# Kernel tuning notes

Measured on AMD Instinct MI355X. Metric: run time of the kernel, lower is better.

Reference implementation:

```python
import jax, jax.numpy as jnp
import numpy as np

N, K, D = 8192, 256, 64

def setup_inputs() -> dict:
    key = jax.random.key(0)
    k1, k2, k3, k4, k5 = jax.random.split(key, 5)
    x = jax.random.normal(k1, (N, D), dtype=jnp.float32)
    means = 0.001 * jax.random.uniform(k2, (K, D), dtype=jnp.float32)
    diag = jax.random.normal(k3, (1, K, D), dtype=jnp.float32)
    tri = 0.01 * jax.random.normal(k4, (1, K, D, D), dtype=jnp.float32)
    weigh = jax.random.normal(k5, (1, K), dtype=jnp.float32)
    return {"x": x, "means": means, "diag": diag, "tri": tri, "weigh": weigh}

def reference(x, means, diag, tri, weigh):
    d = x.shape[1]
    logC = -d / 2 * jnp.log(jnp.asarray(2 * np.pi, dtype=x.dtype))
    w = jax.nn.log_softmax(weigh, axis=1)                 # [1,K]
    y = x[:, None, :] - means[None, :, :]                 # [N,K,d]
    lv = jnp.tanh(diag)                                   # [1,K,d]
    y = y * lv                                            # [N,K,d]
    L = jnp.tril(tri[0], k=-1)                            # [K,d,d] strictly lower
    y = y + jnp.einsum('kij,nkj->nki', L, y)              # [N,K,d]
    q = jnp.sum(y * y, axis=2)                            # [N,K]
    logdet = jnp.sum(jnp.log(jnp.abs(lv)), axis=2)        # [1,K]
    val = -q / 2 + logdet + w                             # [N,K]
    logpdf = logC + jax.nn.logsumexp(val, axis=-1)        # [N]
    return jnp.mean(-logpdf)                              # scalar
```

## Files before the change

kernel.cpp:

```cpp
#include <hip/hip_runtime.h>
#include <cstdint>
#include <cstddef>

#define NTOT 8192
#define KTOT 256

typedef _Float16 half2v __attribute__((ext_vector_type(2)));
typedef _Float16 half8  __attribute__((ext_vector_type(8)));
typedef float floatx16 __attribute__((ext_vector_type(16)));

static constexpr size_t G_ELEMS   = (size_t)8 * 260 * 64 * 8;
static constexpr size_t OFF_CK    = G_ELEMS * 2;
static constexpr size_t OFF_BPART = OFF_CK + 1024;
static constexpr size_t OFF_VAL   = 2134016;

__device__ __forceinline__ uint16_t f2h(float x) {
  _Float16 h = (_Float16)x;
  return __builtin_bit_cast(uint16_t, h);
}

__device__ __forceinline__ half8 mkh(half2v s, const half2v* rp) {
  union { half2v p[4]; half8 v; } u;
  u.p[0] = s * rp[0]; u.p[1] = s * rp[1]; u.p[2] = s * rp[2]; u.p[3] = s * rp[3];
  return u.v;
}
__device__ __forceinline__ half8 cph(const half2v* rp) {
  union { half2v p[4]; half8 v; } u;
  u.p[0] = rp[0]; u.p[1] = rp[1]; u.p[2] = rp[2]; u.p[3] = rp[3];
  return u.v;
}

__global__ void p1_prep(const float* __restrict__ means, const float* __restrict__ diag,
                        const float* __restrict__ tri, const float* __restrict__ weigh,
                        uint16_t* __restrict__ Gf, float* __restrict__ ck) {
  int k = blockIdx.x;
  int t = threadIdx.x;
  __shared__ float lv[64], ms[64], bv64[64], wred[256];
  __shared__ float Wp[64][68];
  __shared__ float SS[64][65];
  __shared__ float lse_s;

  float wv = weigh[t];
  wred[t] = wv; __syncthreads();
  for (int o = 128; o > 0; o >>= 1) { if (t < o) wred[t] = fmaxf(wred[t], wred[t + o]); __syncthreads(); }
  float wm = wred[0]; __syncthreads();
  wred[t] = __expf(wv - wm); __syncthreads();
  for (int o = 128; o > 0; o >>= 1) { if (t < o) wred[t] += wred[t + o]; __syncthreads(); }
  if (t == 0) lse_s = wm + __logf(wred[0]);

  float logdet0 = 0.f;
  if (t < 64) {
    float d = diag[k * 64 + t];
    float l = tanhf(d);
    lv[t] = l;
    ms[t] = means[k * 64 + t];
    float ld = __logf(fabsf(l));
    #pragma unroll
    for (int o = 32; o > 0; o >>= 1) ld += __shfl_xor(ld, o);
    logdet0 = ld;
  }
  __syncthreads();

  for (int e = 0; e < 16; ++e) {
    int idx = e * 256 + t;
    int i = idx >> 6, c = idx & 63;
    float L = (c < i) ? tri[k * 4096 + idx] : 0.f;
    float w = ((c == i) ? 1.f : 0.f) + L;
    Wp[i][c] = w * lv[c];
  }
  __syncthreads();

  int i0 = (t >> 4) * 4, j0 = (t & 15) * 4;
  float acc[4][4];
  #pragma unroll
  for (int a = 0; a < 4; ++a)
    #pragma unroll
    for (int b = 0; b < 4; ++b) acc[a][b] = 0.f;
  for (int r = 0; r < 64; ++r) {
    float4 av = *(const float4*)&Wp[r][i0];
    float4 bv = *(const float4*)&Wp[r][j0];
    float aa[4] = {av.x, av.y, av.z, av.w};
    float bb[4] = {bv.x, bv.y, bv.z, bv.w};
    #pragma unroll
    for (int a = 0; a < 4; ++a)
      #pragma unroll
      for (int b = 0; b < 4; ++b) acc[a][b] = fmaf(aa[a], bb[b], acc[a][b]);
  }
  #pragma unroll
  for (int a = 0; a < 4; ++a)
    #pragma unroll
    for (int b = 0; b < 4; ++b) SS[i0 + a][j0 + b] = acc[a][b];
  __syncthreads();

  if (t < 64) {
    float b = 0.f;
    for (int j = 0; j < 64; ++j) b = fmaf(SS[t][j], ms[j], b);
    bv64[t] = b;
    float bm = b * ms[t];
    #pragma unroll
    for (int o = 32; o > 0; o >>= 1) bm += __shfl_xor(bm, o);
    if (t == 0) ck[k] = logdet0 + (weigh[k] - lse_s) - 0.5f * bm;
  }
  __syncthreads();

  int k32 = k >> 5, kl = k & 31;
  for (int cc = t; cc < 520; cc += 256) {
    float v[8];
    if (cc < 512) {
      int i = cc >> 3, jb = (cc & 7) * 8;
      #pragma unroll
      for (int e = 0; e < 8; ++e) v[e] = -0.5f * SS[i][jb + e];
    } else {
      int b0 = (cc - 512) * 8;
      #pragma unroll
      for (int e = 0; e < 8; ++e) v[e] = bv64[b0 + e];
    }
    uint4 pk;
    pk.x = (uint32_t)f2h(v[0]) | ((uint32_t)f2h(v[1]) << 16);
    pk.y = (uint32_t)f2h(v[2]) | ((uint32_t)f2h(v[3]) << 16);
    pk.z = (uint32_t)f2h(v[4]) | ((uint32_t)f2h(v[5]) << 16);
    pk.w = (uint32_t)f2h(v[6]) | ((uint32_t)f2h(v[7]) << 16);
    size_t base = ((size_t)(k32 * 260 + (cc >> 1)) * 64 + (cc & 1) * 32 + kl) * 8;
    *(uint4*)(Gf + base) = pk;
  }
}

__launch_bounds__(256)
__global__ void k2_gemm(const float* __restrict__ x, const uint16_t* __restrict__ Gf,
                        const float* __restrict__ ck, float* __restrict__ val2) {
  __shared__ float xl[128][65];
  int t = threadIdx.x;
  int bx = blockIdx.x, by = blockIdx.y;
  const float* xblk = x + (size_t)bx * (128 * 64);

  for (int e = 0; e < 8; ++e) {
    int lin = e * 1024 + t * 4;
    float4 v = *(const float4*)(xblk + lin);
    int r = lin >> 6, c = lin & 63;
    xl[r][c] = v.x; xl[r][c + 1] = v.y; xl[r][c + 2] = v.z; xl[r][c + 3] = v.w;
  }
  __syncthreads();

  int wave = t >> 6, l = t & 63;
  int wn = wave >> 1, wk = wave & 1;
  int half = l >> 5, lane31 = l & 31;
  int r0 = wn * 64 + lane31, r1 = r0 + 32;

  half2v runh0[4][4], runh1[4][4];
  #pragma unroll
  for (int c = 0; c < 4; ++c) {
    int base = c * 16 + half * 8;
    float4 ra = *(const float4*)(xblk + (size_t)r0 * 64 + base);
    float4 rb = *(const float4*)(xblk + (size_t)r0 * 64 + base + 4);
    runh0[c][0][0] = (_Float16)ra.x; runh0[c][0][1] = (_Float16)ra.y;
    runh0[c][1][0] = (_Float16)ra.z; runh0[c][1][1] = (_Float16)ra.w;
    runh0[c][2][0] = (_Float16)rb.x; runh0[c][2][1] = (_Float16)rb.y;
    runh0[c][3][0] = (_Float16)rb.z; runh0[c][3][1] = (_Float16)rb.w;
    float4 rc = *(const float4*)(xblk + (size_t)r1 * 64 + base);
    float4 rd = *(const float4*)(xblk + (size_t)r1 * 64 + base + 4);
    runh1[c][0][0] = (_Float16)rc.x; runh1[c][0][1] = (_Float16)rc.y;
    runh1[c][1][0] = (_Float16)rc.z; runh1[c][1][1] = (_Float16)rc.w;
    runh1[c][2][0] = (_Float16)rd.x; runh1[c][2][1] = (_Float16)rd.y;
    runh1[c][3][0] = (_Float16)rd.z; runh1[c][3][1] = (_Float16)rd.w;
  }

  int k32 = by * 2 + wk;
  const uint4* Bp = (const uint4*)Gf;
  size_t bofs = (size_t)(k32 * 260) * 64 + l;

  floatx16 acc0, acc1;
  #pragma unroll
  for (int i = 0; i < 16; ++i) { acc0[i] = 0.f; acc1[i] = 0.f; }

  uint4 bufs[4][4];
  #pragma unroll
  for (int p = 0; p < 4; ++p)
    #pragma unroll
    for (int c = 0; c < 4; ++c) bufs[p][c] = Bp[bofs + (size_t)(p * 4 + c) * 64];

  for (int g = 0; g < 64; g += 4) {
    #pragma unroll
    for (int p = 0; p < 4; ++p) {
      int gg = g + p;
      float xf0 = xl[r0][gg], xf1 = xl[r1][gg];
      _Float16 h0 = (_Float16)xf0; half2v xi0; xi0[0] = h0; xi0[1] = h0;
      _Float16 h1 = (_Float16)xf1; half2v xi1; xi1[0] = h1; xi1[1] = h1;
      #pragma unroll
      for (int c = 0; c < 4; ++c) {
        half8 a0 = mkh(xi0, runh0[c]);
        half8 a1 = mkh(xi1, runh1[c]);
        half8 bb = __builtin_bit_cast(half8, bufs[p][c]);
        acc0 = __builtin_amdgcn_mfma_f32_32x32x16_f16(a0, bb, acc0, 0, 0, 0);
        acc1 = __builtin_amdgcn_mfma_f32_32x32x16_f16(a1, bb, acc1, 0, 0, 0);
      }
      #pragma unroll
      for (int c = 0; c < 4; ++c)
        bufs[p][c] = Bp[bofs + (size_t)((gg + 4) * 4 + c) * 64];
    }
  }

  #pragma unroll
  for (int c = 0; c < 4; ++c) {
    half8 a0 = cph(runh0[c]);
    half8 a1 = cph(runh1[c]);
    half8 bb = __builtin_bit_cast(half8, bufs[0][c]);
    acc0 = __builtin_amdgcn_mfma_f32_32x32x16_f16(a0, bb, acc0, 0, 0, 0);
    acc1 = __builtin_amdgcn_mfma_f32_32x32x16_f16(a1, bb, acc1, 0, 0, 0);
  }

  __syncthreads();
  float ckv = ck[by * 64 + wk * 32 + lane31];
  #pragma unroll
  for (int reg = 0; reg < 16; ++reg) {
    int row = (reg & 3) + 8 * (reg >> 2) + 4 * half;
    xl[wn * 64 + row][wk * 32 + lane31] = acc0[reg] + ckv;
    xl[wn * 64 + 32 + row][wk * 32 + lane31] = acc1[reg] + ckv;
  }
  __syncthreads();
  if (t < 128) {
    float m = -3.0e38f;
    #pragma unroll
    for (int j = 0; j < 64; ++j) m = fmaxf(m, xl[t][j]);
    float s = 0.f;
    #pragma unroll
    for (int j = 0; j < 64; ++j) s += __expf(xl[t][j] - m);
    size_t n = (size_t)bx * 128 + t;
    val2[n * 8 + by * 2 + 0] = m;
    val2[n * 8 + by * 2 + 1] = s;
  }
}

__global__ void k3_lse(const float* __restrict__ val2, float* __restrict__ bpart) {
  __shared__ float red[4];
  int t = threadIdx.x;
  size_t n = (size_t)blockIdx.x * 256 + t;
  const float4* p = (const float4*)(val2 + n * 8);
  float4 a = p[0], b = p[1];
  float M = fmaxf(fmaxf(a.x, a.z), fmaxf(b.x, b.z));
  float s = a.y * __expf(a.x - M) + a.w * __expf(a.z - M) +
            b.y * __expf(b.x - M) + b.w * __expf(b.z - M);
  float lse = M + __logf(s);
  #pragma unroll
  for (int o = 32; o > 0; o >>= 1) lse += __shfl_xor(lse, o);
  if ((t & 63) == 0) red[t >> 6] = lse;
  __syncthreads();
  if (t == 0) bpart[blockIdx.x] = red[0] + red[1] + red[2] + red[3];
}

__global__ void k4_final(const float* __restrict__ bpart, float* __restrict__ out) {
  int t = threadIdx.x;
  float v = (t < 32) ? bpart[t] : 0.f;
  #pragma unroll
  for (int o = 32; o > 0; o >>= 1) v += __shfl_xor(v, o);
  if (t == 0) out[0] = 58.8120661251f - v / 8192.0f;
}

extern "C" void kernel_launch(void* const* d_in, const int* in_sizes, int n_in,
                              void* d_out, int out_size, void* d_ws, size_t ws_size,
                              hipStream_t stream) {
  const float* x     = (const float*)d_in[0];
  const float* means = (const float*)d_in[1];
  const float* diag  = (const float*)d_in[2];
  const float* tri   = (const float*)d_in[3];
  const float* weigh = (const float*)d_in[4];

  char* ws = (char*)d_ws;
  uint16_t* Gf  = (uint16_t*)ws;
  float* ck     = (float*)(ws + OFF_CK);
  float* bpart  = (float*)(ws + OFF_BPART);
  float* val2   = (float*)(ws + OFF_VAL);

  p1_prep<<<dim3(256), dim3(256), 0, stream>>>(means, diag, tri, weigh, Gf, ck);
  k2_gemm<<<dim3(64, 4), dim3(256), 0, stream>>>(x, Gf, ck, val2);
  k3_lse<<<dim3(32), dim3(256), 0, stream>>>(val2, bpart);
  k4_final<<<dim3(1), dim3(64), 0, stream>>>(bpart, (float*)d_out);
}
```

Measured before the change: 97.95 us.

## Fuse all four kernels into one cooperative kernel with grid sync and last-block reduction

Merges the prep, GEMM/logsumexp, per-row LSE and final reduction kernels into a single cooperative launch of 256 blocks. A grid-wide sync separates the parameter preparation from the GEMM phase. A ticketed atomic counter lets the last finishing block do the final reduction. This removes three kernel launches and their inter-kernel gaps, at the cost of grid-sync overhead and higher LDS use per block, since both stages' shared arrays now coexist. The counter is reset by block 0 within the same launch, which relies on ordering that the grid sync provides.

After: 160.1 us. 1.64x slower.

```diff
diff --git a/kernel.cpp b/kernel.cpp
--- a/kernel.cpp
+++ b/kernel.cpp
@@ -1,6 +1,9 @@
 #include <hip/hip_runtime.h>
+#include <hip/hip_cooperative_groups.h>
 #include <cstdint>
 #include <cstddef>
+
+namespace cg = cooperative_groups;
 
 #define NTOT 8192
 #define KTOT 256
@@ -11,7 +14,7 @@
 
 static constexpr size_t G_ELEMS   = (size_t)8 * 260 * 64 * 8;
 static constexpr size_t OFF_CK    = G_ELEMS * 2;
-static constexpr size_t OFF_BPART = OFF_CK + 1024;
+static constexpr size_t OFF_CNT   = OFF_CK + 1024;
 static constexpr size_t OFF_VAL   = 2134016;
 
 __device__ __forceinline__ uint16_t f2h(float x) {
@@ -30,229 +33,237 @@
   return u.v;
 }
 
-__global__ void p1_prep(const float* __restrict__ means, const float* __restrict__ diag,
-                        const float* __restrict__ tri, const float* __restrict__ weigh,
-                        uint16_t* __restrict__ Gf, float* __restrict__ ck) {
-  int k = blockIdx.x;
-  int t = threadIdx.x;
+__launch_bounds__(256)
+__global__ void fused(const float* __restrict__ x, const float* __restrict__ means,
+                      const float* __restrict__ diag, const float* __restrict__ tri,
+                      const float* __restrict__ weigh, uint16_t* __restrict__ Gf,
+                      float* __restrict__ ck, float* __restrict__ val2,
+                      unsigned int* __restrict__ counter, float* __restrict__ out) {
   __shared__ float lv[64], ms[64], bv64[64], wred[256];
   __shared__ float Wp[64][68];
   __shared__ float SS[64][65];
   __shared__ float lse_s;
-
-  float wv = weigh[t];
-  wred[t] = wv; __syncthreads();
-  for (int o = 128; o > 0; o >>= 1) { if (t < o) wred[t] = fmaxf(wred[t], wred[t + o]); __syncthreads(); }
-  float wm = wred[0]; __syncthreads();
-  wred[t] = __expf(wv - wm); __syncthreads();
-  for (int o = 128; o > 0; o >>= 1) { if (t < o) wred[t] += wred[t + o]; __syncthreads(); }
-  if (t == 0) lse_s = wm + __logf(wred[0]);
-
-  float logdet0 = 0.f;
-  if (t < 64) {
-    float d = diag[k * 64 + t];
-    float l = tanhf(d);
-    lv[t] = l;
-    ms[t] = means[k * 64 + t];
-    float ld = __logf(fabsf(l));
-    #pragma unroll
-    for (int o = 32; o > 0; o >>= 1) ld += __shfl_xor(ld, o);
-    logdet0 = ld;
+  __shared__ float xl[128][65];
+  __shared__ int ticket_s;
+
+  int t = threadIdx.x;
+
+  {
+    int k = blockIdx.x;
+    if (k == 0 && t == 0) *counter = 0;
+
+    float wv = weigh[t];
+    wred[t] = wv; __syncthreads();
+    for (int o = 128; o > 0; o >>= 1) { if (t < o) wred[t] = fmaxf(wred[t], wred[t + o]); __syncthreads(); }
+    float wm = wred[0]; __syncthreads();
+    wred[t] = __expf(wv - wm); __syncthreads();
+    for (int o = 128; o > 0; o >>= 1) { if (t < o) wred[t] += wred[t + o]; __syncthreads(); }
+    if (t == 0) lse_s = wm + __logf(wred[0]);
+
+    float logdet0 = 0.f;
+    if (t < 64) {
+      float d = diag[k * 64 + t];
+      float l = tanhf(d);
+      lv[t] = l;
+      ms[t] = means[k * 64 + t];
+      float ld = __logf(fabsf(l));
+      #pragma unroll
+      for (int o = 32; o > 0; o >>= 1) ld += __shfl_xor(ld, o);
+      logdet0 = ld;
+    }
+    __syncthreads();
+
+    for (int e = 0; e < 16; ++e) {
+      int idx = e * 256 + t;
+      int i = idx >> 6, c = idx & 63;
+      float L = (c < i) ? tri[k * 4096 + idx] : 0.f;
+      float w = ((c == i) ? 1.f : 0.f) + L;
+      Wp[i][c] = w * lv[c];
+    }
+    __syncthreads();
+
+    int i0 = (t >> 4) * 4, j0 = (t & 15) * 4;
+    float acc[4][4];
+    #pragma unroll
+    for (int a = 0; a < 4; ++a)
+      #pragma unroll
+      for (int b = 0; b < 4; ++b) acc[a][b] = 0.f;
+    for (int r = 0; r < 64; ++r) {
+      float4 av = *(const float4*)&Wp[r][i0];
+      float4 bv = *(const float4*)&Wp[r][j0];
+      float aa[4] = {av.x, av.y, av.z, av.w};
+      float bb[4] = {bv.x, bv.y, bv.z, bv.w};
+      #pragma unroll
+      for (int a = 0; a < 4; ++a)
+        #pragma unroll
+        for (int b = 0; b < 4; ++b) acc[a][b] = fmaf(aa[a], bb[b], acc[a][b]);
+    }
+    #pragma unroll
+    for (int a = 0; a < 4; ++a)
+      #pragma unroll
+      for (int b = 0; b < 4; ++b) SS[i0 + a][j0 + b] = acc[a][b];
+    __syncthreads();
+
+    if (t < 64) {
+      float b = 0.f;
+      for (int j = 0; j < 64; ++j) b = fmaf(SS[t][j], ms[j], b);
+      bv64[t] = b;
+      float bm = b * ms[t];
+      #pragma unroll
+      for (int o = 32; o > 0; o >>= 1) bm += __shfl_xor(bm, o);
+      if (t == 0) ck[k] = logdet0 + (weigh[k] - lse_s) - 0.5f * bm;
+    }
+    __syncthreads();
+
+    int k32 = k >> 5, kl = k & 31;
+    for (int cc = t; cc < 520; cc += 256) {
+      float v[8];
+      if (cc < 512) {
+        int i = cc >> 3, jb = (cc & 7) * 8;
+        #pragma unroll
+        for (int e = 0; e < 8; ++e) v[e] = -0.5f * SS[i][jb + e];
+      } else {
+        int b0 = (cc - 512) * 8;
+        #pragma unroll
+        for (int e = 0; e < 8; ++e) v[e] = bv64[b0 + e];
+      }
+      uint4 pk;
+      pk.x = (uint32_t)f2h(v[0]) | ((uint32_t)f2h(v[1]) << 16);
+      pk.y = (uint32_t)f2h(v[2]) | ((uint32_t)f2h(v[3]) << 16);
+      pk.z = (uint32_t)f2h(v[4]) | ((uint32_t)f2h(v[5]) << 16);
+      pk.w = (uint32_t)f2h(v[6]) | ((uint32_t)f2h(v[7]) << 16);
+      size_t base = ((size_t)(k32 * 260 + (cc >> 1)) * 64 + (cc & 1) * 32 + kl) * 8;
+      *(uint4*)(Gf + base) = pk;
+    }
+  }
+
+  cg::this_grid().sync();
+
+  {
+    int bx = blockIdx.x >> 2, by = blockIdx.x & 3;
+    const float* xblk = x + (size_t)bx * (128 * 64);
+
+    for (int e = 0; e < 8; ++e) {
+      int lin = e * 1024 + t * 4;
+      float4 v = *(const float4*)(xblk + lin);
+      int r = lin >> 6, c = lin & 63;
+      xl[r][c] = v.x; xl[r][c + 1] = v.y; xl[r][c + 2] = v.z; xl[r][c + 3] = v.w;
+    }
+    __syncthreads();
+
+    int wave = t >> 6, l = t & 63;
+    int wn = wave >> 1, wk = wave & 1;
+    int half = l >> 5, lane31 = l & 31;
+    int r0 = wn * 64 + lane31, r1 = r0 + 32;
+
+    half2v runh0[4][4], runh1[4][4];
+    #pragma unroll
+    for (int c = 0; c < 4; ++c) {
+      int base = c * 16 + half * 8;
+      float4 ra = *(const float4*)(xblk + (size_t)r0 * 64 + base);
+      float4 rb = *(const float4*)(xblk + (size_t)r0 * 64 + base + 4);
+      runh0[c][0][0] = (_Float16)ra.x; runh0[c][0][1] = (_Float16)ra.y;
+      runh0[c][1][0] = (_Float16)ra.z; runh0[c][1][1] = (_Float16)ra.w;
+      runh0[c][2][0] = (_Float16)rb.x; runh0[c][2][1] = (_Float16)rb.y;
+      runh0[c][3][0] = (_Float16)rb.z; runh0[c][3][1] = (_Float16)rb.w;
+      float4 rc = *(const float4*)(xblk + (size_t)r1 * 64 + base);
+      float4 rd = *(const float4*)(xblk + (size_t)r1 * 64 + base + 4);
+      runh1[c][0][0] = (_Float16)rc.x; runh1[c][0][1] = (_Float16)rc.y;
+      runh1[c][1][0] = (_Float16)rc.z; runh1[c][1][1] = (_Float16)rc.w;
+      runh1[c][2][0] = (_Float16)rd.x; runh1[c][2][1] = (_Float16)rd.y;
+      runh1[c][3][0] = (_Float16)rd.z; runh1[c][3][1] = (_Float16)rd.w;
+    }
+
+    int k32 = by * 2 + wk;
+    const uint4* Bp = (const uint4*)Gf;
+    size_t bofs = (size_t)(k32 * 260) * 64 + l;
+
+    floatx16 acc0, acc1;
+    #pragma unroll
+    for (int i = 0; i < 16; ++i) { acc0[i] = 0.f; acc1[i] = 0.f; }
+
+    uint4 bufs[4][4];
+    #pragma unroll
+    for (int p = 0; p < 4; ++p)
+      #pragma unroll
+      for (int c = 0; c < 4; ++c) bufs[p][c] = Bp[bofs + (size_t)(p * 4 + c) * 64];
+
+    for (int g = 0; g < 64; g += 4) {
+      #pragma unroll
+      for (int p = 0; p < 4; ++p) {
+        int gg = g + p;
+        float xf0 = xl[r0][gg], xf1 = xl[r1][gg];
+        _Float16 h0 = (_Float16)xf0; half2v xi0; xi0[0] = h0; xi0[1] = h0;
+        _Float16 h1 = (_Float16)xf1; half2v xi1; xi1[0] = h1; xi1[1] = h1;
+        #pragma unroll
+        for (int c = 0; c < 4; ++c) {
+          half8 a0 = mkh(xi0, runh0[c]);
+          half8 a1 = mkh(xi1, runh1[c]);
+          half8 bb = __builtin_bit_cast(half8, bufs[p][c]);
+          acc0 = __builtin_amdgcn_mfma_f32_32x32x16_f16(a0, bb, acc0, 0, 0, 0);
+          acc1 = __builtin_amdgcn_mfma_f32_32x32x16_f16(a1, bb, acc1, 0, 0, 0);
+        }
+        #pragma unroll
+        for (int c = 0; c < 4; ++c)
+          bufs[p][c] = Bp[bofs + (size_t)((gg + 4) * 4 + c) * 64];
+      }
+    }
+
+    #pragma unroll
+    for (int c = 0; c < 4; ++c) {
+      half8 a0 = cph(runh0[c]);
+      half8 a1 = cph(runh1[c]);
+      half8 bb = __builtin_bit_cast(half8, bufs[0][c]);
+      acc0 = __builtin_amdgcn_mfma_f32_32x32x16_f16(a0, bb, acc0, 0, 0, 0);
+      acc1 = __builtin_amdgcn_mfma_f32_32x32x16_f16(a1, bb, acc1, 0, 0, 0);
+    }
+
+    __syncthreads();
+    float ckv = ck[by * 64 + wk * 32 + lane31];
+    #pragma unroll
+    for (int reg = 0; reg < 16; ++reg) {
+      int row = (reg & 3) + 8 * (reg >> 2) + 4 * half;
+      xl[wn * 64 + row][wk * 32 + lane31] = acc0[reg] + ckv;
+      xl[wn * 64 + 32 + row][wk * 32 + lane31] = acc1[reg] + ckv;
+    }
+    __syncthreads();
+    if (t < 128) {
+      float m = -3.0e38f;
+      #pragma unroll
+      for (int j = 0; j < 64; ++j) m = fmaxf(m, xl[t][j]);
+      float s = 0.f;
+      #pragma unroll
+      for (int j = 0; j < 64; ++j) s += __expf(xl[t][j] - m);
+      size_t n = (size_t)bx * 128 + t;
+      val2[n * 8 + by * 2 + 0] = m;
+      val2[n * 8 + by * 2 + 1] = s;
+    }
+    __syncthreads();
+  }
+
+  if (t == 0) {
+    __threadfence();
+    ticket_s = (int)atomicAdd(counter, 1u);
   }
   __syncthreads();
-
-  for (int e = 0; e < 16; ++e) {
-    int idx = e * 256 + t;
-    int i = idx >> 6, c = idx & 63;
-    float L = (c < i) ? tri[k * 4096 + idx] : 0.f;
-    float w = ((c == i) ? 1.f : 0.f) + L;
-    Wp[i][c] = w * lv[c];
-  }
-  __syncthreads();
-
-  int i0 = (t >> 4) * 4, j0 = (t & 15) * 4;
-  float acc[4][4];
-  #pragma unroll
-  for (int a = 0; a < 4; ++a)
-    #pragma unroll
-    for (int b = 0; b < 4; ++b) acc[a][b] = 0.f;
-  for (int r = 0; r < 64; ++r) {
-    float4 av = *(const float4*)&Wp[r][i0];
-    float4 bv = *(const float4*)&Wp[r][j0];
-    float aa[4] = {av.x, av.y, av.z, av.w};
-    float bb[4] = {bv.x, bv.y, bv.z, bv.w};
-    #pragma unroll
-    for (int a = 0; a < 4; ++a)
-      #pragma unroll
-      for (int b = 0; b < 4; ++b) acc[a][b] = fmaf(aa[a], bb[b], acc[a][b]);
-  }
-  #pragma unroll
-  for (int a = 0; a < 4; ++a)
-    #pragma unroll
-    for (int b = 0; b < 4; ++b) SS[i0 + a][j0 + b] = acc[a][b];
-  __syncthreads();
-
-  if (t < 64) {
-    float b = 0.f;
-    for (int j = 0; j < 64; ++j) b = fmaf(SS[t][j], ms[j], b);
-    bv64[t] = b;
-    float bm = b * ms[t];
-    #pragma unroll
-    for (int o = 32; o > 0; o >>= 1) bm += __shfl_xor(bm, o);
-    if (t == 0) ck[k] = logdet0 + (weigh[k] - lse_s) - 0.5f * bm;
-  }
-  __syncthreads();
-
-  int k32 = k >> 5, kl = k & 31;
-  for (int cc = t; cc < 520; cc += 256) {
-    float v[8];
-    if (cc < 512) {
-      int i = cc >> 3, jb = (cc & 7) * 8;
-      #pragma unroll
-      for (int e = 0; e < 8; ++e) v[e] = -0.5f * SS[i][jb + e];
-    } else {
-      int b0 = (cc - 512) * 8;
-      #pragma unroll
-      for (int e = 0; e < 8; ++e) v[e] = bv64[b0 + e];
-    }
-    uint4 pk;
-    pk.x = (uint32_t)f2h(v[0]) | ((uint32_t)f2h(v[1]) << 16);
-    pk.y = (uint32_t)f2h(v[2]) | ((uint32_t)f2h(v[3]) << 16);
-    pk.z = (uint32_t)f2h(v[4]) | ((uint32_t)f2h(v[5]) << 16);
-    pk.w = (uint32_t)f2h(v[6]) | ((uint32_t)f2h(v[7]) << 16);
-    size_t base = ((size_t)(k32 * 260 + (cc >> 1)) * 64 + (cc & 1) * 32 + kl) * 8;
-    *(uint4*)(Gf + base) = pk;
-  }
-}
-
-__launch_bounds__(256)
-__global__ void k2_gemm(const float* __restrict__ x, const uint16_t* __restrict__ Gf,
-                        const float* __restrict__ ck, float* __restrict__ val2) {
-  __shared__ float xl[128][65];
-  int t = threadIdx.x;
-  int bx = blockIdx.x, by = blockIdx.y;
-  const float* xblk = x + (size_t)bx * (128 * 64);
-
-  for (int e = 0; e < 8; ++e) {
-    int lin = e * 1024 + t * 4;
-    float4 v = *(const float4*)(xblk + lin);
-    int r = lin >> 6, c = lin & 63;
-    xl[r][c] = v.x; xl[r][c + 1] = v.y; xl[r][c + 2] = v.z; xl[r][c + 3] = v.w;
-  }
-  __syncthreads();
-
-  int wave = t >> 6, l = t & 63;
-  int wn = wave >> 1, wk = wave & 1;
-  int half = l >> 5, lane31 = l & 31;
-  int r0 = wn * 64 + lane31, r1 = r0 + 32;
-
-  half2v runh0[4][4], runh1[4][4];
-  #pragma unroll
-  for (int c = 0; c < 4; ++c) {
-    int base = c * 16 + half * 8;
-    float4 ra = *(const float4*)(xblk + (size_t)r0 * 64 + base);
-    float4 rb = *(const float4*)(xblk + (size_t)r0 * 64 + base + 4);
-    runh0[c][0][0] = (_Float16)ra.x; runh0[c][0][1] = (_Float16)ra.y;
-    runh0[c][1][0] = (_Float16)ra.z; runh0[c][1][1] = (_Float16)ra.w;
-    runh0[c][2][0] = (_Float16)rb.x; runh0[c][2][1] = (_Float16)rb.y;
-    runh0[c][3][0] = (_Float16)rb.z; runh0[c][3][1] = (_Float16)rb.w;
-    float4 rc = *(const float4*)(xblk + (size_t)r1 * 64 + base);
-    float4 rd = *(const float4*)(xblk + (size_t)r1 * 64 + base + 4);
-    runh1[c][0][0] = (_Float16)rc.x; runh1[c][0][1] = (_Float16)rc.y;
-    runh1[c][1][0] = (_Float16)rc.z; runh1[c][1][1] = (_Float16)rc.w;
-    runh1[c][2][0] = (_Float16)rd.x; runh1[c][2][1] = (_Float16)rd.y;
-    runh1[c][3][0] = (_Float16)rd.z; runh1[c][3][1] = (_Float16)rd.w;
-  }
-
-  int k32 = by * 2 + wk;
-  const uint4* Bp = (const uint4*)Gf;
-  size_t bofs = (size_t)(k32 * 260) * 64 + l;
-
-  floatx16 acc0, acc1;
-  #pragma unroll
-  for (int i = 0; i < 16; ++i) { acc0[i] = 0.f; acc1[i] = 0.f; }
-
-  uint4 bufs[4][4];
-  #pragma unroll
-  for (int p = 0; p < 4; ++p)
-    #pragma unroll
-    for (int c = 0; c < 4; ++c) bufs[p][c] = Bp[bofs + (size_t)(p * 4 + c) * 64];
-
-  for (int g = 0; g < 64; g += 4) {
-    #pragma unroll
-    for (int p = 0; p < 4; ++p) {
-      int gg = g + p;
-      float xf0 = xl[r0][gg], xf1 = xl[r1][gg];
-      _Float16 h0 = (_Float16)xf0; half2v xi0; xi0[0] = h0; xi0[1] = h0;
-      _Float16 h1 = (_Float16)xf1; half2v xi1; xi1[0] = h1; xi1[1] = h1;
-      #pragma unroll
-      for (int c = 0; c < 4; ++c) {
-        half8 a0 = mkh(xi0, runh0[c]);
-        half8 a1 = mkh(xi1, runh1[c]);
-        half8 bb = __builtin_bit_cast(half8, bufs[p][c]);
-        acc0 = __builtin_amdgcn_mfma_f32_32x32x16_f16(a0, bb, acc0, 0, 0, 0);
-        acc1 = __builtin_amdgcn_mfma_f32_32x32x16_f16(a1, bb, acc1, 0, 0, 0);
-      }
-      #pragma unroll
-      for (int c = 0; c < 4; ++c)
-        bufs[p][c] = Bp[bofs + (size_t)((gg + 4) * 4 + c) * 64];
-    }
-  }
-
-  #pragma unroll
-  for (int c = 0; c < 4; ++c) {
-    half8 a0 = cph(runh0[c]);
-    half8 a1 = cph(runh1[c]);
-    half8 bb = __builtin_bit_cast(half8, bufs[0][c]);
-    acc0 = __builtin_amdgcn_mfma_f32_32x32x16_f16(a0, bb, acc0, 0, 0, 0);
-    acc1 = __builtin_amdgcn_mfma_f32_32x32x16_f16(a1, bb, acc1, 0, 0, 0);
-  }
-
-  __syncthreads();
-  float ckv = ck[by * 64 + wk * 32 + lane31];
-  #pragma unroll
-  for (int reg = 0; reg < 16; ++reg) {
-    int row = (reg & 3) + 8 * (reg >> 2) + 4 * half;
-    xl[wn * 64 + row][wk * 32 + lane31] = acc0[reg] + ckv;
-    xl[wn * 64 + 32 + row][wk * 32 + lane31] = acc1[reg] + ckv;
-  }
-  __syncthreads();
-  if (t < 128) {
-    float m = -3.0e38f;
-    #pragma unroll
-    for (int j = 0; j < 64; ++j) m = fmaxf(m, xl[t][j]);
-    float s = 0.f;
-    #pragma unroll
-    for (int j = 0; j < 64; ++j) s += __expf(xl[t][j] - m);
-    size_t n = (size_t)bx * 128 + t;
-    val2[n * 8 + by * 2 + 0] = m;
-    val2[n * 8 + by * 2 + 1] = s;
-  }
-}
-
-__global__ void k3_lse(const float* __restrict__ val2, float* __restrict__ bpart) {
-  __shared__ float red[4];
-  int t = threadIdx.x;
-  size_t n = (size_t)blockIdx.x * 256 + t;
-  const float4* p = (const float4*)(val2 + n * 8);
-  float4 a = p[0], b = p[1];
-  float M = fmaxf(fmaxf(a.x, a.z), fmaxf(b.x, b.z));
-  float s = a.y * __expf(a.x - M) + a.w * __expf(a.z - M) +
-            b.y * __expf(b.x - M) + b.w * __expf(b.z - M);
-  float lse = M + __logf(s);
-  #pragma unroll
-  for (int o = 32; o > 0; o >>= 1) lse += __shfl_xor(lse, o);
-  if ((t & 63) == 0) red[t >> 6] = lse;
-  __syncthreads();
-  if (t == 0) bpart[blockIdx.x] = red[0] + red[1] + red[2] + red[3];
-}
-
-__global__ void k4_final(const float* __restrict__ bpart, float* __restrict__ out) {
-  int t = threadIdx.x;
-  float v = (t < 32) ? bpart[t] : 0.f;
-  #pragma unroll
-  for (int o = 32; o > 0; o >>= 1) v += __shfl_xor(v, o);
-  if (t == 0) out[0] = 58.8120661251f - v / 8192.0f;
+  if (ticket_s == 255) {
+    __threadfence();
+    float acc = 0.f;
+    #pragma unroll 4
+    for (int i = 0; i < 32; ++i) {
+      size_t n = (size_t)i * 256 + t;
+      const float4* p = (const float4*)(val2 + n * 8);
+      float4 a = p[0], b = p[1];
+      float M = fmaxf(fmaxf(a.x, a.z), fmaxf(b.x, b.z));
+      float s = a.y * __expf(a.x - M) + a.w * __expf(a.z - M) +
+                b.y * __expf(b.x - M) + b.w * __expf(b.z - M);
+      acc += M + __logf(s);
+    }
+    __syncthreads();
+    wred[t] = acc; __syncthreads();
+    for (int o = 128; o > 0; o >>= 1) { if (t < o) wred[t] += wred[t + o]; __syncthreads(); }
+    if (t == 0) out[0] = 58.8120661251f - wred[0] / 8192.0f;
+  }
 }
 
 extern "C" void kernel_launch(void* const* d_in, const int* in_sizes, int n_in,
@@ -265,13 +276,13 @@
   const float* weigh = (const float*)d_in[4];
 
   char* ws = (char*)d_ws;
-  uint16_t* Gf  = (uint16_t*)ws;
-  float* ck     = (float*)(ws + OFF_CK);
-  float* bpart  = (float*)(ws + OFF_BPART);
-  float* val2   = (float*)(ws + OFF_VAL);
-
-  p1_prep<<<dim3(256), dim3(256), 0, stream>>>(means, diag, tri, weigh, Gf, ck);
-  k2_gemm<<<dim3(64, 4), dim3(256), 0, stream>>>(x, Gf, ck, val2);
-  k3_lse<<<dim3(32), dim3(256), 0, stream>>>(val2, bpart);
-  k4_final<<<dim3(1), dim3(64), 0, stream>>>(bpart, (float*)d_out);
-}
+  uint16_t* Gf          = (uint16_t*)ws;
+  float* ck             = (float*)(ws + OFF_CK);
+  unsigned int* counter = (unsigned int*)(ws + OFF_CNT);
+  float* val2           = (float*)(ws + OFF_VAL);
+  float* out            = (float*)d_out;
+
+  void* args[] = { (void*)&x, (void*)&means, (void*)&diag, (void*)&tri, (void*)&weigh,
+                   (void*)&Gf, (void*)&ck, (void*)&val2, (void*)&counter, (void*)&out };
+  hipLaunchCooperativeKernel((void*)fused, dim3(256), dim3(256), args, 0, stream);
+}
```
